# Kernel optimization log

Hardware: AMD Instinct MI355X
Metric: run time of the kernel (lower is better)

## Reference

```python
import jax, jax.numpy as jnp
import numpy as np

N, E, D, G = 50000, 600000, 128, 1024
NEG_SLOPE = 0.2  # PyG GATConv default negative_slope


def setup_inputs() -> dict:
    key = jax.random.key(0)
    ks = jax.random.split(key, 20)
    s = 1.0 / np.sqrt(D)
    inp = {
        "x": jax.random.normal(ks[0], (N, D), jnp.float32),
        "edge_index": jax.random.randint(ks[1], (2, E), 0, N, dtype=jnp.int64),
        "edge_attr": jax.random.normal(ks[2], (E, 1), jnp.float32),  # ignored (edge_dim=None)
        "batch": jnp.sort(jax.random.randint(ks[3], (N,), 0, G, dtype=jnp.int64)),
    }
    k = 4
    for name in ("g1", "g2", "g3"):
        inp[f"{name}_W"] = jax.random.normal(ks[k], (D, D), jnp.float32) * s; k += 1
        inp[f"{name}_a_src"] = jax.random.normal(ks[k], (D,), jnp.float32) * s; k += 1
        inp[f"{name}_a_dst"] = jax.random.normal(ks[k], (D,), jnp.float32) * s; k += 1
        inp[f"{name}_b"] = jnp.zeros((D,), jnp.float32)
    inp["lin_W"] = jax.random.normal(ks[k], (D, D), jnp.float32) * s
    inp["lin_b"] = jnp.zeros((D,), jnp.float32)
    return inp


def _gat(x, src, dst, W, a_src, a_dst, b):
    # PyG GATConv, heads=1: project, edge attention logits, scatter-softmax over
    # destination nodes, weighted scatter-add aggregation, plus bias.
    n = x.shape[0]
    h = x @ W                                            # [N, D]
    logits = jax.nn.leaky_relu((h @ a_src)[src] + (h @ a_dst)[dst], NEG_SLOPE)  # [E']
    m = jax.ops.segment_max(logits, dst, num_segments=n)
    p = jnp.exp(logits - m[dst])
    denom = jax.ops.segment_sum(p, dst, num_segments=n)
    alpha = p / (denom[dst] + 1e-16)                     # PyG softmax eps
    out = jax.ops.segment_sum(alpha[:, None] * h[src], dst, num_segments=n)
    return out + b


def reference(x, edge_index, edge_attr, batch,
              g1_W, g1_a_src, g1_a_dst, g1_b,
              g2_W, g2_a_src, g2_a_dst, g2_b,
              g3_W, g3_a_src, g3_a_dst, g3_b,
              lin_W, lin_b):
    n = x.shape[0]
    # GATConv default add_self_loops=True
    loop = jnp.arange(n, dtype=edge_index.dtype)
    src = jnp.concatenate([edge_index[0], loop])
    dst = jnp.concatenate([edge_index[1], loop])

    h = jax.nn.relu(_gat(x, src, dst, g1_W, g1_a_src, g1_a_dst, g1_b))
    h = jax.nn.relu(_gat(h, src, dst, g2_W, g2_a_src, g2_a_dst, g2_b))
    h = _gat(h, src, dst, g3_W, g3_a_src, g3_a_dst, g3_b)

    # global_mean_pool over graph ids
    sums = jax.ops.segment_sum(h, batch, num_segments=G)
    cnts = jax.ops.segment_sum(jnp.ones((n,), h.dtype), batch, num_segments=G)
    pooled = sums / jnp.maximum(cnts, 1.0)[:, None]
    # dropout(p=0.5) is identity in eval mode
    return pooled @ lin_W + lin_b
```

## Files before the change

### kernel.cpp

```cpp
#include <hip/hip_runtime.h>

#define D 128
typedef unsigned short ushort_t;
typedef __attribute__((ext_vector_type(8))) short bf16x8;
typedef __attribute__((ext_vector_type(4))) float f32x4;

__device__ __forceinline__ float wred_max(float v){
#pragma unroll
  for (int o = 1; o < 64; o <<= 1) v = fmaxf(v, __shfl_xor(v, o, 64));
  return v;
}
__device__ __forceinline__ float wred_sum(float v){
#pragma unroll
  for (int o = 1; o < 64; o <<= 1) v += __shfl_xor(v, o, 64);
  return v;
}
__device__ __forceinline__ unsigned short f2bf(float f){
  unsigned u = __float_as_uint(f);
  unsigned r = (u + 0x7FFFu + ((u >> 16) & 1u)) >> 16;
  return (unsigned short)r;
}
__device__ __forceinline__ float bflo(unsigned u){ return __uint_as_float(u << 16); }
__device__ __forceinline__ float bfhi(unsigned u){ return __uint_as_float(u & 0xFFFF0000u); }

__global__ __launch_bounds__(256) void k_init(const float* __restrict__ W0,
                                              const float* __restrict__ W1,
                                              const float* __restrict__ W2,
                                              ushort_t* __restrict__ Wp,
                                              int* __restrict__ cnt, int n){
  int b = blockIdx.x;
  if (b < 192){
    int wi = b >> 6;
    const float* W = wi == 0 ? W0 : (wi == 1 ? W1 : W2);
    ushort_t* dst = Wp + wi * 16384;
    int idx = (b & 63) * 256 + threadIdx.x;
    int k = idx >> 7, c = idx & 127;
    int ct = c >> 4, s = k >> 5, lane = (c & 15) | (((k >> 3) & 3) << 4), e = k & 7;
    dst[((ct * 4 + s) * 64 + lane) * 8 + e] = f2bf(W[idx]);
  } else {
    int i = (b - 192) * 256 + threadIdx.x;
    if (i < n) cnt[i] = 0;
  }
}

template<bool XF32>
__device__ __forceinline__ void gemm_body(int bid, const void* __restrict__ Av,
                                          const ushort_t* __restrict__ Wp,
                                          const float* __restrict__ a_src,
                                          const float* __restrict__ a_dst,
                                          ushort_t* __restrict__ Hbf,
                                          float* __restrict__ as_,
                                          float* __restrict__ ad_,
                                          int n){
  int tid = threadIdx.x;
  int wid = tid >> 6, l = tid & 63;
  int kg = l >> 4, cin = l & 15;
  int r0 = bid * 64 + wid * 16;
  int row_l = r0 + cin;
  if (row_l > n - 1) row_l = n - 1;

  bf16x8 ah[4], al[4];
  if (XF32){
    const float* xp = (const float*)Av + (size_t)row_l * D + kg * 8;
#pragma unroll
    for (int s = 0; s < 4; s++){
      float4 f0 = *(const float4*)(xp + s * 32);
      float4 f1 = *(const float4*)(xp + s * 32 + 4);
      float fv[8] = {f0.x, f0.y, f0.z, f0.w, f1.x, f1.y, f1.z, f1.w};
#pragma unroll
      for (int e = 0; e < 8; e++){
        unsigned short h = f2bf(fv[e]);
        ah[s][e] = (short)h;
        float r = fv[e] - __uint_as_float((unsigned)h << 16);
        al[s][e] = (short)f2bf(r);
      }
    }
  } else {
    const ushort_t* xp = (const ushort_t*)Av + (size_t)row_l * D + kg * 8;
#pragma unroll
    for (int s = 0; s < 4; s++) ah[s] = *(const bf16x8*)(xp + s * 32);
  }

  const bf16x8* Bh = (const bf16x8*)Wp;

  f32x4 acc[8];
#pragma unroll
  for (int ct = 0; ct < 8; ct++) acc[ct] = (f32x4){0.f, 0.f, 0.f, 0.f};

#pragma unroll
  for (int ct = 0; ct < 8; ct++)
#pragma unroll
    for (int s = 0; s < 4; s++){
      bf16x8 bh = Bh[(ct * 4 + s) * 64 + l];
      acc[ct] = __builtin_amdgcn_mfma_f32_16x16x32_bf16(ah[s], bh, acc[ct], 0, 0, 0);
      if (XF32)
        acc[ct] = __builtin_amdgcn_mfma_f32_16x16x32_bf16(al[s], bh, acc[ct], 0, 0, 0);
    }

  float asv[8], adv[8];
#pragma unroll
  for (int ct = 0; ct < 8; ct++){
    asv[ct] = a_src[ct * 16 + cin];
    adv[ct] = a_dst[ct * 16 + cin];
  }
#pragma unroll
  for (int j = 0; j < 4; j++){
    float ps = 0.f, pd = 0.f;
#pragma unroll
    for (int ct = 0; ct < 8; ct++){ ps += acc[ct][j] * asv[ct]; pd += acc[ct][j] * adv[ct]; }
#pragma unroll
    for (int o = 1; o < 16; o <<= 1){ ps += __shfl_xor(ps, o, 64); pd += __shfl_xor(pd, o, 64); }
    int row = r0 + kg * 4 + j;
    if (row < n){
      if (cin == 0) as_[row] = ps;
      if (cin == 1) ad_[row] = pd;
#pragma unroll
      for (int ct = 0; ct < 8; ct++)
        Hbf[(size_t)row * D + ct * 16 + cin] = f2bf(acc[ct][j]);
    }
  }
}

__global__ __launch_bounds__(256) void k_gemm_mfma_bf(const void* __restrict__ Av,
                                                      const ushort_t* __restrict__ Wp,
                                                      const float* __restrict__ a_src,
                                                      const float* __restrict__ a_dst,
                                                      ushort_t* __restrict__ Hbf,
                                                      float* __restrict__ as_,
                                                      float* __restrict__ ad_,
                                                      int n){
  gemm_body<false>(blockIdx.x, Av, Wp, a_src, a_dst, Hbf, as_, ad_, n);
}

__global__ __launch_bounds__(256) void k_gemm1_fill(const float* __restrict__ x,
                                                    const ushort_t* __restrict__ Wp,
                                                    const float* __restrict__ a_src,
                                                    const float* __restrict__ a_dst,
                                                    ushort_t* __restrict__ Hbf,
                                                    float* __restrict__ as_,
                                                    float* __restrict__ ad_,
                                                    int n, int gemm_grid,
                                                    const int* __restrict__ src,
                                                    const int* __restrict__ dst,
                                                    int E, int sliceN,
                                                    int* __restrict__ cnt,
                                                    ushort_t* __restrict__ csr_pad){
  int b = blockIdx.x;
  if (b < gemm_grid){
    gemm_body<true>(b, x, Wp, a_src, a_dst, Hbf, as_, ad_, n);
  } else {
    int f = b - gemm_grid;
    int chunk = f >> 3;
    int slice = b & 7;
    int d_lo = slice * sliceN;
    int d_hi = d_lo + sliceN;
    int e0 = chunk * 2048 + (int)threadIdx.x;
#pragma unroll
    for (int i = 0; i < 8; i++){
      int e = e0 + i * 256;
      if (e < E){
        int d = dst[e];
        if (d >= d_lo && d < d_hi){
          int s = src[e];
          int slot = atomicAdd(&cnt[d], 1);
          if (slot < 63) csr_pad[((size_t)d << 6) + slot] = (ushort_t)s;
        }
      }
    }
  }
}

template<bool OUTBF>
__global__ __launch_bounds__(256) void k_agg(const uint4* __restrict__ hb4,
                                             const ushort_t* __restrict__ csr_pad,
                                             const int* __restrict__ cnt,
                                             const float* __restrict__ asrc,
                                             const float* __restrict__ adst,
                                             const float* __restrict__ bias,
                                             ushort_t* __restrict__ outb,
                                             float* __restrict__ outf,
                                             int relu, int n){
  int node = (blockIdx.x * 256 + threadIdx.x) >> 6;
  if (node >= n) return;
  int lane = threadIdx.x & 63;
  int q = lane & 15, g = lane >> 4;
  int degr = cnt[node]; if (degr > 63) degr = 63;
  int degp = degr + 1;
  const ushort_t* eb = csr_pad + ((size_t)node << 6);
  float adn = adst[node];

  int s = node; float logit = -1e30f;
  if (lane < degr) s = eb[lane];
  if (lane <= degr){
    float xx = asrc[s] + adn;
    logit = xx >= 0.f ? xx : 0.2f * xx;
  }
  float m = wred_max(logit);
  float p = (lane <= degr) ? __expf(logit - m) : 0.f;
  float denom = wred_sum(p);
  float inv = 1.f / (denom + 1e-16f);

  float acc[8] = {0.f, 0.f, 0.f, 0.f, 0.f, 0.f, 0.f, 0.f};
#pragma unroll 2
  for (int j = 0; j < degp; j += 4){
    int slot = j + g;
    int   sj = __shfl(s, slot, 64);
    float wj = (slot < degp) ? __shfl(p, slot, 64) : 0.f;
    uint4 v = hb4[(size_t)sj * 16 + q];
    acc[0] += wj * bflo(v.x); acc[1] += wj * bfhi(v.x);
    acc[2] += wj * bflo(v.y); acc[3] += wj * bfhi(v.y);
    acc[4] += wj * bflo(v.z); acc[5] += wj * bfhi(v.z);
    acc[6] += wj * bflo(v.w); acc[7] += wj * bfhi(v.w);
  }
#pragma unroll
  for (int o = 16; o < 64; o <<= 1){
#pragma unroll
    for (int i = 0; i < 8; i++) acc[i] += __shfl_xor(acc[i], o, 64);
  }

  if (g == 0){
    float4 b0 = *(const float4*)&bias[q * 8];
    float4 b1 = *(const float4*)&bias[q * 8 + 4];
    float o0 = acc[0] * inv + b0.x, o1 = acc[1] * inv + b0.y;
    float o2 = acc[2] * inv + b0.z, o3 = acc[3] * inv + b0.w;
    float o4 = acc[4] * inv + b1.x, o5 = acc[5] * inv + b1.y;
    float o6 = acc[6] * inv + b1.z, o7 = acc[7] * inv + b1.w;
    if (relu){
      o0 = fmaxf(o0, 0.f); o1 = fmaxf(o1, 0.f); o2 = fmaxf(o2, 0.f); o3 = fmaxf(o3, 0.f);
      o4 = fmaxf(o4, 0.f); o5 = fmaxf(o5, 0.f); o6 = fmaxf(o6, 0.f); o7 = fmaxf(o7, 0.f);
    }
    if (OUTBF){
      ushort4 u0, u1;
      u0.x = f2bf(o0); u0.y = f2bf(o1); u0.z = f2bf(o2); u0.w = f2bf(o3);
      u1.x = f2bf(o4); u1.y = f2bf(o5); u1.z = f2bf(o6); u1.w = f2bf(o7);
      *(ushort4*)&outb[(size_t)node * D + q * 8]     = u0;
      *(ushort4*)&outb[(size_t)node * D + q * 8 + 4] = u1;
    } else {
      *(float4*)&outf[(size_t)node * D + q * 8]     = make_float4(o0, o1, o2, o3);
      *(float4*)&outf[(size_t)node * D + q * 8 + 4] = make_float4(o4, o5, o6, o7);
    }
  }
}

__device__ __forceinline__ int lbound(const int* a, int n, int key){
  int lo = 0, hi = n;
  while (lo < hi){ int mid = (lo + hi) >> 1; if (a[mid] < key) lo = mid + 1; else hi = mid; }
  return lo;
}

__global__ __launch_bounds__(128) void k_pool_final(const float* __restrict__ x,
                                                    const int* __restrict__ batch,
                                                    const float* __restrict__ Wl,
                                                    const float* __restrict__ bl,
                                                    float* __restrict__ out, int n){
  __shared__ float pl[128];
  int g = blockIdx.x;
  int c = threadIdx.x;
  int lo = lbound(batch, n, g);
  int hi = lbound(batch, n, g + 1);
  float sum = 0.f;
  for (int i = lo; i < hi; i++) sum += x[(size_t)i * D + c];
  float cnt = (float)(hi - lo);
  pl[c] = sum / fmaxf(cnt, 1.f);
  __syncthreads();
  float acc = bl[c];
#pragma unroll 4
  for (int k = 0; k < 128; k++) acc += pl[k] * Wl[(size_t)k * D + c];
  out[(size_t)g * D + c] = acc;
}

extern "C" void kernel_launch(void* const* d_in, const int* in_sizes, int n_in,
                              void* d_out, int out_size, void* d_ws, size_t ws_size,
                              hipStream_t stream){
  const float* x     = (const float*)d_in[0];
  const int*   ei    = (const int*)d_in[1];
  const int*   batch = (const int*)d_in[3];
  const float* gW[3]  = {(const float*)d_in[4],  (const float*)d_in[8],  (const float*)d_in[12]};
  const float* gAs[3] = {(const float*)d_in[5],  (const float*)d_in[9],  (const float*)d_in[13]};
  const float* gAd[3] = {(const float*)d_in[6],  (const float*)d_in[10], (const float*)d_in[14]};
  const float* gB[3]  = {(const float*)d_in[7],  (const float*)d_in[11], (const float*)d_in[15]};
  const float* linW = (const float*)d_in[16];
  const float* linB = (const float*)d_in[17];
  float* outp = (float*)d_out;

  int N  = in_sizes[3];
  int E  = in_sizes[1] / 2;
  int G  = out_size / D;

  char* ws = (char*)d_ws;
  size_t off = 0;
  auto alloc = [&](size_t bytes)->void*{
    void* p = ws + off;
    off += (bytes + 255) & ~(size_t)255;
    return p;
  };
  float*    bufF    = (float*)alloc((size_t)N * D * 4);
  ushort_t* bufB    = (ushort_t*)alloc((size_t)N * D * 2);
  ushort_t* Hbf     = (ushort_t*)alloc((size_t)N * D * 2);
  float*    as_     = (float*)alloc((size_t)N * 4);
  float*    ad_     = (float*)alloc((size_t)N * 4);
  int*      cnt     = (int*)  alloc((size_t)N * 4);
  ushort_t* csr_pad = (ushort_t*)alloc((size_t)N * 64 * 2);
  ushort_t* Wp      = (ushort_t*)alloc(3 * 16384 * 2);
  (void)ws_size; (void)n_in;

  const int* esrc = ei;
  const int* edst = ei + E;

  int tpb = 256;
  int ngrid = (N + tpb - 1) / tpb;
  int gemm_grid = (N + 63) / 64;
  int node_grid = (N + 3) / 4;
  int nchunk = (E + 2047) / 2048;
  int sliceN = (N + 7) / 8;

  k_init<<<192 + ngrid, tpb, 0, stream>>>(gW[0], gW[1], gW[2], Wp, cnt, N);

  const uint4* hbu = (const uint4*)Hbf;

  k_gemm1_fill<<<gemm_grid + nchunk * 8, tpb, 0, stream>>>(x, Wp, gAs[0], gAd[0], Hbf, as_, ad_, N,
                                                           gemm_grid, esrc, edst, E, sliceN, cnt, csr_pad);
  k_agg<true>  <<<node_grid, tpb, 0, stream>>>(hbu, csr_pad, cnt, as_, ad_, gB[0], bufB, nullptr, 1, N);
  k_gemm_mfma_bf<<<gemm_grid, tpb, 0, stream>>>(bufB, Wp + 16384, gAs[1], gAd[1], Hbf, as_, ad_, N);
  k_agg<true>  <<<node_grid, tpb, 0, stream>>>(hbu, csr_pad, cnt, as_, ad_, gB[1], bufB, nullptr, 1, N);
  k_gemm_mfma_bf<<<gemm_grid, tpb, 0, stream>>>(bufB, Wp + 32768, gAs[2], gAd[2], Hbf, as_, ad_, N);
  k_agg<false> <<<node_grid, tpb, 0, stream>>>(hbu, csr_pad, cnt, as_, ad_, gB[2], nullptr, bufF, 0, N);

  k_pool_final<<<G, 128, 0, stream>>>(bufF, batch, linW, linB, outp, N);
}
```

Baseline: 211.1 us.

## Reorder GAT to aggregate-then-project and fuse aggregation with GEMM

Precomputes W·a_src and W·a_dst so attention logits can be computed from layer inputs, then aggregates neighbour features before multiplying by W inside a single fused per-layer kernel. This removes the separate GEMM launches and the intermediate H buffer writes/reads, and emits next-layer logits in the epilogue. In exchange, layer 1 gathers fp32 rows (double bytes), the GEMM uses a 3-pass split-bf16 scheme, and the large shared-memory tile with serial per-wave node loops may reduce occupancy.

```diff
diff --git a/kernel.cpp b/kernel.cpp
--- a/kernel.cpp
+++ b/kernel.cpp
@@ -22,134 +22,79 @@
 }
 __device__ __forceinline__ float bflo(unsigned u){ return __uint_as_float(u << 16); }
 __device__ __forceinline__ float bfhi(unsigned u){ return __uint_as_float(u & 0xFFFF0000u); }
+__device__ __forceinline__ int lbound(const int* a, int n, int key){
+  int lo = 0, hi = n;
+  while (lo < hi){ int mid = (lo + hi) >> 1; if (a[mid] < key) lo = mid + 1; else hi = mid; }
+  return lo;
+}
 
 __global__ __launch_bounds__(256) void k_init(const float* __restrict__ W0,
                                               const float* __restrict__ W1,
                                               const float* __restrict__ W2,
+                                              const float* __restrict__ As0, const float* __restrict__ Ad0,
+                                              const float* __restrict__ As1, const float* __restrict__ Ad1,
+                                              const float* __restrict__ As2, const float* __restrict__ Ad2,
                                               ushort_t* __restrict__ Wp,
+                                              float* __restrict__ wv,
                                               int* __restrict__ cnt, int n){
   int b = blockIdx.x;
   if (b < 192){
     int wi = b >> 6;
     const float* W = wi == 0 ? W0 : (wi == 1 ? W1 : W2);
-    ushort_t* dst = Wp + wi * 16384;
+    ushort_t* dst = Wp + wi * 32768;
     int idx = (b & 63) * 256 + threadIdx.x;
     int k = idx >> 7, c = idx & 127;
+    float w = W[idx];
+    unsigned short hi = f2bf(w);
+    float r = w - __uint_as_float((unsigned)hi << 16);
     int ct = c >> 4, s = k >> 5, lane = (c & 15) | (((k >> 3) & 3) << 4), e = k & 7;
-    dst[((ct * 4 + s) * 64 + lane) * 8 + e] = f2bf(W[idx]);
+    int off = ((ct * 4 + s) * 64 + lane) * 8 + e;
+    dst[off] = hi;
+    dst[16384 + off] = f2bf(r);
+  } else if (b < 198){
+    int vi = b - 192;
+    int li = vi >> 1;
+    const float* W = li == 0 ? W0 : (li == 1 ? W1 : W2);
+    const float* a = (vi & 1) ? (li == 0 ? Ad0 : (li == 1 ? Ad1 : Ad2))
+                              : (li == 0 ? As0 : (li == 1 ? As1 : As2));
+    int t = threadIdx.x;
+    if (t < 128){
+      float acc = 0.f;
+#pragma unroll 4
+      for (int c = 0; c < 128; c++) acc += W[(size_t)t * D + c] * a[c];
+      wv[vi * 128 + t] = acc;
+    }
   } else {
-    int i = (b - 192) * 256 + threadIdx.x;
+    int i = (b - 198) * 256 + threadIdx.x;
     if (i < n) cnt[i] = 0;
   }
 }
 
-template<bool XF32>
-__device__ __forceinline__ void gemm_body(int bid, const void* __restrict__ Av,
-                                          const ushort_t* __restrict__ Wp,
-                                          const float* __restrict__ a_src,
-                                          const float* __restrict__ a_dst,
-                                          ushort_t* __restrict__ Hbf,
-                                          float* __restrict__ as_,
-                                          float* __restrict__ ad_,
-                                          int n){
-  int tid = threadIdx.x;
-  int wid = tid >> 6, l = tid & 63;
-  int kg = l >> 4, cin = l & 15;
-  int r0 = bid * 64 + wid * 16;
-  int row_l = r0 + cin;
-  if (row_l > n - 1) row_l = n - 1;
-
-  bf16x8 ah[4], al[4];
-  if (XF32){
-    const float* xp = (const float*)Av + (size_t)row_l * D + kg * 8;
-#pragma unroll
-    for (int s = 0; s < 4; s++){
-      float4 f0 = *(const float4*)(xp + s * 32);
-      float4 f1 = *(const float4*)(xp + s * 32 + 4);
-      float fv[8] = {f0.x, f0.y, f0.z, f0.w, f1.x, f1.y, f1.z, f1.w};
-#pragma unroll
-      for (int e = 0; e < 8; e++){
-        unsigned short h = f2bf(fv[e]);
-        ah[s][e] = (short)h;
-        float r = fv[e] - __uint_as_float((unsigned)h << 16);
-        al[s][e] = (short)f2bf(r);
-      }
-    }
+__global__ __launch_bounds__(256) void k_fill_dots(const float* __restrict__ x,
+                                                   const float* __restrict__ wv,
+                                                   float* __restrict__ asA,
+                                                   float* __restrict__ adA,
+                                                   int n, int dgrid,
+                                                   const int* __restrict__ src,
+                                                   const int* __restrict__ dst,
+                                                   int E, int sliceN,
+                                                   int* __restrict__ cnt,
+                                                   ushort_t* __restrict__ csr_pad){
+  int b = blockIdx.x;
+  if (b < dgrid){
+    int w = (b * 256 + (int)threadIdx.x) >> 6;
+    if (w >= n) return;
+    int lane = threadIdx.x & 63;
+    float2 hv = *(const float2*)&x[(size_t)w * D + lane * 2];
+    float2 s2 = *(const float2*)&wv[lane * 2];
+    float2 d2 = *(const float2*)&wv[128 + lane * 2];
+    float ps = hv.x * s2.x + hv.y * s2.y;
+    float pd = hv.x * d2.x + hv.y * d2.y;
+#pragma unroll
+    for (int o = 1; o < 64; o <<= 1){ ps += __shfl_xor(ps, o, 64); pd += __shfl_xor(pd, o, 64); }
+    if (lane == 0){ asA[w] = ps; adA[w] = pd; }
   } else {
-    const ushort_t* xp = (const ushort_t*)Av + (size_t)row_l * D + kg * 8;
-#pragma unroll
-    for (int s = 0; s < 4; s++) ah[s] = *(const bf16x8*)(xp + s * 32);
-  }
-
-  const bf16x8* Bh = (const bf16x8*)Wp;
-
-  f32x4 acc[8];
-#pragma unroll
-  for (int ct = 0; ct < 8; ct++) acc[ct] = (f32x4){0.f, 0.f, 0.f, 0.f};
-
-#pragma unroll
-  for (int ct = 0; ct < 8; ct++)
-#pragma unroll
-    for (int s = 0; s < 4; s++){
-      bf16x8 bh = Bh[(ct * 4 + s) * 64 + l];
-      acc[ct] = __builtin_amdgcn_mfma_f32_16x16x32_bf16(ah[s], bh, acc[ct], 0, 0, 0);
-      if (XF32)
-        acc[ct] = __builtin_amdgcn_mfma_f32_16x16x32_bf16(al[s], bh, acc[ct], 0, 0, 0);
-    }
-
-  float asv[8], adv[8];
-#pragma unroll
-  for (int ct = 0; ct < 8; ct++){
-    asv[ct] = a_src[ct * 16 + cin];
-    adv[ct] = a_dst[ct * 16 + cin];
-  }
-#pragma unroll
-  for (int j = 0; j < 4; j++){
-    float ps = 0.f, pd = 0.f;
-#pragma unroll
-    for (int ct = 0; ct < 8; ct++){ ps += acc[ct][j] * asv[ct]; pd += acc[ct][j] * adv[ct]; }
-#pragma unroll
-    for (int o = 1; o < 16; o <<= 1){ ps += __shfl_xor(ps, o, 64); pd += __shfl_xor(pd, o, 64); }
-    int row = r0 + kg * 4 + j;
-    if (row < n){
-      if (cin == 0) as_[row] = ps;
-      if (cin == 1) ad_[row] = pd;
-#pragma unroll
-      for (int ct = 0; ct < 8; ct++)
-        Hbf[(size_t)row * D + ct * 16 + cin] = f2bf(acc[ct][j]);
-    }
-  }
-}
-
-__global__ __launch_bounds__(256) void k_gemm_mfma_bf(const void* __restrict__ Av,
-                                                      const ushort_t* __restrict__ Wp,
-                                                      const float* __restrict__ a_src,
-                                                      const float* __restrict__ a_dst,
-                                                      ushort_t* __restrict__ Hbf,
-                                                      float* __restrict__ as_,
-                                                      float* __restrict__ ad_,
-                                                      int n){
-  gemm_body<false>(blockIdx.x, Av, Wp, a_src, a_dst, Hbf, as_, ad_, n);
-}
-
-__global__ __launch_bounds__(256) void k_gemm1_fill(const float* __restrict__ x,
-                                                    const ushort_t* __restrict__ Wp,
-                                                    const float* __restrict__ a_src,
-                                                    const float* __restrict__ a_dst,
-                                                    ushort_t* __restrict__ Hbf,
-                                                    float* __restrict__ as_,
-                                                    float* __restrict__ ad_,
-                                                    int n, int gemm_grid,
-                                                    const int* __restrict__ src,
-                                                    const int* __restrict__ dst,
-                                                    int E, int sliceN,
-                                                    int* __restrict__ cnt,
-                                                    ushort_t* __restrict__ csr_pad){
-  int b = blockIdx.x;
-  if (b < gemm_grid){
-    gemm_body<true>(b, x, Wp, a_src, a_dst, Hbf, as_, ad_, n);
-  } else {
-    int f = b - gemm_grid;
+    int f = b - dgrid;
     int chunk = f >> 3;
     int slice = b & 7;
     int d_lo = slice * sliceN;
@@ -170,82 +115,145 @@
   }
 }
 
-template<bool OUTBF>
-__global__ __launch_bounds__(256) void k_agg(const uint4* __restrict__ hb4,
-                                             const ushort_t* __restrict__ csr_pad,
-                                             const int* __restrict__ cnt,
-                                             const float* __restrict__ asrc,
-                                             const float* __restrict__ adst,
-                                             const float* __restrict__ bias,
-                                             ushort_t* __restrict__ outb,
-                                             float* __restrict__ outf,
-                                             int relu, int n){
-  int node = (blockIdx.x * 256 + threadIdx.x) >> 6;
-  if (node >= n) return;
-  int lane = threadIdx.x & 63;
-  int q = lane & 15, g = lane >> 4;
-  int degr = cnt[node]; if (degr > 63) degr = 63;
-  int degp = degr + 1;
-  const ushort_t* eb = csr_pad + ((size_t)node << 6);
-  float adn = adst[node];
-
-  int s = node; float logit = -1e30f;
-  if (lane < degr) s = eb[lane];
-  if (lane <= degr){
-    float xx = asrc[s] + adn;
-    logit = xx >= 0.f ? xx : 0.2f * xx;
-  }
-  float m = wred_max(logit);
-  float p = (lane <= degr) ? __expf(logit - m) : 0.f;
-  float denom = wred_sum(p);
-  float inv = 1.f / (denom + 1e-16f);
-
-  float acc[8] = {0.f, 0.f, 0.f, 0.f, 0.f, 0.f, 0.f, 0.f};
+template<int MODE>
+__global__ __launch_bounds__(256) void k_layer(const void* __restrict__ Xin,
+                                               const ushort_t* __restrict__ Wp,
+                                               const float* __restrict__ as_cur,
+                                               const float* __restrict__ ad_cur,
+                                               const float* __restrict__ wv_next,
+                                               const float* __restrict__ bias,
+                                               ushort_t* __restrict__ outb,
+                                               float* __restrict__ outf,
+                                               float* __restrict__ as_next,
+                                               float* __restrict__ ad_next,
+                                               const ushort_t* __restrict__ csr_pad,
+                                               const int* __restrict__ cnt, int n){
+  __shared__ float zsh[64][132];
+  int tid = (int)threadIdx.x;
+  int w = tid >> 6, l = tid & 63;
+  int q = l & 15, g = l >> 4;
+  int nb0 = blockIdx.x * 64;
+
+  for (int i = 0; i < 16; i++){
+    int node = nb0 + w * 16 + i;
+    float acc[8] = {0.f, 0.f, 0.f, 0.f, 0.f, 0.f, 0.f, 0.f};
+    float inv = 0.f;
+    if (node < n){
+      int degr = cnt[node]; if (degr > 63) degr = 63;
+      int degp = degr + 1;
+      const ushort_t* eb = csr_pad + ((size_t)node << 6);
+      float adn = ad_cur[node];
+      int s = node; float logit = -1e30f;
+      if (l < degr) s = eb[l];
+      if (l <= degr){
+        float xx = as_cur[s] + adn;
+        logit = xx >= 0.f ? xx : 0.2f * xx;
+      }
+      float m = wred_max(logit);
+      float p = (l <= degr) ? __expf(logit - m) : 0.f;
+      float denom = wred_sum(p);
+      inv = 1.f / (denom + 1e-16f);
 #pragma unroll 2
-  for (int j = 0; j < degp; j += 4){
-    int slot = j + g;
-    int   sj = __shfl(s, slot, 64);
-    float wj = (slot < degp) ? __shfl(p, slot, 64) : 0.f;
-    uint4 v = hb4[(size_t)sj * 16 + q];
-    acc[0] += wj * bflo(v.x); acc[1] += wj * bfhi(v.x);
-    acc[2] += wj * bflo(v.y); acc[3] += wj * bfhi(v.y);
-    acc[4] += wj * bflo(v.z); acc[5] += wj * bfhi(v.z);
-    acc[6] += wj * bflo(v.w); acc[7] += wj * bfhi(v.w);
-  }
-#pragma unroll
-  for (int o = 16; o < 64; o <<= 1){
-#pragma unroll
-    for (int i = 0; i < 8; i++) acc[i] += __shfl_xor(acc[i], o, 64);
-  }
-
-  if (g == 0){
-    float4 b0 = *(const float4*)&bias[q * 8];
-    float4 b1 = *(const float4*)&bias[q * 8 + 4];
-    float o0 = acc[0] * inv + b0.x, o1 = acc[1] * inv + b0.y;
-    float o2 = acc[2] * inv + b0.z, o3 = acc[3] * inv + b0.w;
-    float o4 = acc[4] * inv + b1.x, o5 = acc[5] * inv + b1.y;
-    float o6 = acc[6] * inv + b1.z, o7 = acc[7] * inv + b1.w;
-    if (relu){
-      o0 = fmaxf(o0, 0.f); o1 = fmaxf(o1, 0.f); o2 = fmaxf(o2, 0.f); o3 = fmaxf(o3, 0.f);
-      o4 = fmaxf(o4, 0.f); o5 = fmaxf(o5, 0.f); o6 = fmaxf(o6, 0.f); o7 = fmaxf(o7, 0.f);
-    }
-    if (OUTBF){
-      ushort4 u0, u1;
-      u0.x = f2bf(o0); u0.y = f2bf(o1); u0.z = f2bf(o2); u0.w = f2bf(o3);
-      u1.x = f2bf(o4); u1.y = f2bf(o5); u1.z = f2bf(o6); u1.w = f2bf(o7);
-      *(ushort4*)&outb[(size_t)node * D + q * 8]     = u0;
-      *(ushort4*)&outb[(size_t)node * D + q * 8 + 4] = u1;
-    } else {
-      *(float4*)&outf[(size_t)node * D + q * 8]     = make_float4(o0, o1, o2, o3);
-      *(float4*)&outf[(size_t)node * D + q * 8 + 4] = make_float4(o4, o5, o6, o7);
-    }
-  }
-}
-
-__device__ __forceinline__ int lbound(const int* a, int n, int key){
-  int lo = 0, hi = n;
-  while (lo < hi){ int mid = (lo + hi) >> 1; if (a[mid] < key) lo = mid + 1; else hi = mid; }
-  return lo;
+      for (int j = 0; j < degp; j += 4){
+        int slot = j + g;
+        int   sj = __shfl(s, slot, 64);
+        float wj = (slot < degp) ? __shfl(p, slot, 64) : 0.f;
+        if (MODE == 0){
+          const float4* xr = (const float4*)Xin + (size_t)sj * 32 + q * 2;
+          float4 v0 = xr[0], v1 = xr[1];
+          acc[0] += wj * v0.x; acc[1] += wj * v0.y; acc[2] += wj * v0.z; acc[3] += wj * v0.w;
+          acc[4] += wj * v1.x; acc[5] += wj * v1.y; acc[6] += wj * v1.z; acc[7] += wj * v1.w;
+        } else {
+          uint4 v = ((const uint4*)Xin)[(size_t)sj * 16 + q];
+          acc[0] += wj * bflo(v.x); acc[1] += wj * bfhi(v.x);
+          acc[2] += wj * bflo(v.y); acc[3] += wj * bfhi(v.y);
+          acc[4] += wj * bflo(v.z); acc[5] += wj * bfhi(v.z);
+          acc[6] += wj * bflo(v.w); acc[7] += wj * bfhi(v.w);
+        }
+      }
+#pragma unroll
+      for (int o = 16; o < 64; o <<= 1){
+#pragma unroll
+        for (int ii = 0; ii < 8; ii++) acc[ii] += __shfl_xor(acc[ii], o, 64);
+      }
+    }
+    if (g == 0){
+      float4 z0 = make_float4(acc[0] * inv, acc[1] * inv, acc[2] * inv, acc[3] * inv);
+      float4 z1 = make_float4(acc[4] * inv, acc[5] * inv, acc[6] * inv, acc[7] * inv);
+      *(float4*)&zsh[w * 16 + i][q * 8]     = z0;
+      *(float4*)&zsh[w * 16 + i][q * 8 + 4] = z1;
+    }
+  }
+  __syncthreads();
+
+  int kg = l >> 4, cin = l & 15;
+  bf16x8 ah[4], al[4];
+#pragma unroll
+  for (int s = 0; s < 4; s++){
+    const float4* zr = (const float4*)&zsh[w * 16 + cin][s * 32 + kg * 8];
+    float4 f0 = zr[0], f1 = zr[1];
+    float fv[8] = {f0.x, f0.y, f0.z, f0.w, f1.x, f1.y, f1.z, f1.w};
+#pragma unroll
+    for (int e = 0; e < 8; e++){
+      unsigned short h = f2bf(fv[e]);
+      ah[s][e] = (short)h;
+      al[s][e] = (short)f2bf(fv[e] - __uint_as_float((unsigned)h << 16));
+    }
+  }
+
+  const bf16x8* Bh = (const bf16x8*)Wp;
+  const bf16x8* Bl = (const bf16x8*)(Wp + 16384);
+  f32x4 accc[8];
+#pragma unroll
+  for (int ct = 0; ct < 8; ct++) accc[ct] = (f32x4){0.f, 0.f, 0.f, 0.f};
+#pragma unroll
+  for (int ct = 0; ct < 8; ct++)
+#pragma unroll
+    for (int s = 0; s < 4; s++){
+      bf16x8 bh = Bh[(ct * 4 + s) * 64 + l];
+      bf16x8 bl = Bl[(ct * 4 + s) * 64 + l];
+      accc[ct] = __builtin_amdgcn_mfma_f32_16x16x32_bf16(ah[s], bh, accc[ct], 0, 0, 0);
+      accc[ct] = __builtin_amdgcn_mfma_f32_16x16x32_bf16(al[s], bh, accc[ct], 0, 0, 0);
+      accc[ct] = __builtin_amdgcn_mfma_f32_16x16x32_bf16(ah[s], bl, accc[ct], 0, 0, 0);
+    }
+
+  float bv[8], wsn[8], wdn[8];
+#pragma unroll
+  for (int ct = 0; ct < 8; ct++){
+    bv[ct] = bias[ct * 16 + cin];
+    if (MODE != 2){
+      wsn[ct] = wv_next[ct * 16 + cin];
+      wdn[ct] = wv_next[128 + ct * 16 + cin];
+    }
+  }
+#pragma unroll
+  for (int j = 0; j < 4; j++){
+    int row = nb0 + w * 16 + kg * 4 + j;
+    float o[8];
+#pragma unroll
+    for (int ct = 0; ct < 8; ct++){
+      float v = accc[ct][j] + bv[ct];
+      if (MODE != 2) v = fmaxf(v, 0.f);
+      o[ct] = v;
+    }
+    if (MODE != 2){
+      float ps = 0.f, pd = 0.f;
+#pragma unroll
+      for (int ct = 0; ct < 8; ct++){ ps += o[ct] * wsn[ct]; pd += o[ct] * wdn[ct]; }
+#pragma unroll
+      for (int of = 1; of < 16; of <<= 1){ ps += __shfl_xor(ps, of, 64); pd += __shfl_xor(pd, of, 64); }
+      if (row < n && cin == 0){ as_next[row] = ps; ad_next[row] = pd; }
+    }
+    if (row < n){
+      if (MODE == 2){
+#pragma unroll
+        for (int ct = 0; ct < 8; ct++) outf[(size_t)row * D + ct * 16 + cin] = o[ct];
+      } else {
+#pragma unroll
+        for (int ct = 0; ct < 8; ct++) outb[(size_t)row * D + ct * 16 + cin] = f2bf(o[ct]);
+      }
+    }
+  }
 }
 
 __global__ __launch_bounds__(128) void k_pool_final(const float* __restrict__ x,
@@ -295,13 +303,18 @@
     return p;
   };
   float*    bufF    = (float*)alloc((size_t)N * D * 4);
-  ushort_t* bufB    = (ushort_t*)alloc((size_t)N * D * 2);
-  ushort_t* Hbf     = (ushort_t*)alloc((size_t)N * D * 2);
-  float*    as_     = (float*)alloc((size_t)N * 4);
-  float*    ad_     = (float*)alloc((size_t)N * 4);
+  ushort_t* X2      = (ushort_t*)alloc((size_t)N * D * 2);
+  ushort_t* X3      = (ushort_t*)alloc((size_t)N * D * 2);
+  float*    asA     = (float*)alloc((size_t)N * 4);
+  float*    adA     = (float*)alloc((size_t)N * 4);
+  float*    asB     = (float*)alloc((size_t)N * 4);
+  float*    adB     = (float*)alloc((size_t)N * 4);
+  float*    asC     = (float*)alloc((size_t)N * 4);
+  float*    adC     = (float*)alloc((size_t)N * 4);
   int*      cnt     = (int*)  alloc((size_t)N * 4);
   ushort_t* csr_pad = (ushort_t*)alloc((size_t)N * 64 * 2);
-  ushort_t* Wp      = (ushort_t*)alloc(3 * 16384 * 2);
+  ushort_t* Wp      = (ushort_t*)alloc(3 * 2 * 16384 * 2);
+  float*    wv      = (float*)alloc(6 * 128 * 4);
   (void)ws_size; (void)n_in;
 
   const int* esrc = ei;
@@ -309,22 +322,21 @@
 
   int tpb = 256;
   int ngrid = (N + tpb - 1) / tpb;
-  int gemm_grid = (N + 63) / 64;
-  int node_grid = (N + 3) / 4;
+  int layer_grid = (N + 63) / 64;
+  int dgrid = (N + 3) / 4;
   int nchunk = (E + 2047) / 2048;
   int sliceN = (N + 7) / 8;
 
-  k_init<<<192 + ngrid, tpb, 0, stream>>>(gW[0], gW[1], gW[2], Wp, cnt, N);
-
-  const uint4* hbu = (const uint4*)Hbf;
-
-  k_gemm1_fill<<<gemm_grid + nchunk * 8, tpb, 0, stream>>>(x, Wp, gAs[0], gAd[0], Hbf, as_, ad_, N,
-                                                           gemm_grid, esrc, edst, E, sliceN, cnt, csr_pad);
-  k_agg<true>  <<<node_grid, tpb, 0, stream>>>(hbu, csr_pad, cnt, as_, ad_, gB[0], bufB, nullptr, 1, N);
-  k_gemm_mfma_bf<<<gemm_grid, tpb, 0, stream>>>(bufB, Wp + 16384, gAs[1], gAd[1], Hbf, as_, ad_, N);
-  k_agg<true>  <<<node_grid, tpb, 0, stream>>>(hbu, csr_pad, cnt, as_, ad_, gB[1], bufB, nullptr, 1, N);
-  k_gemm_mfma_bf<<<gemm_grid, tpb, 0, stream>>>(bufB, Wp + 32768, gAs[2], gAd[2], Hbf, as_, ad_, N);
-  k_agg<false> <<<node_grid, tpb, 0, stream>>>(hbu, csr_pad, cnt, as_, ad_, gB[2], nullptr, bufF, 0, N);
-
+  k_init<<<198 + ngrid, tpb, 0, stream>>>(gW[0], gW[1], gW[2],
+                                          gAs[0], gAd[0], gAs[1], gAd[1], gAs[2], gAd[2],
+                                          Wp, wv, cnt, N);
+  k_fill_dots<<<dgrid + nchunk * 8, tpb, 0, stream>>>(x, wv, asA, adA, N, dgrid,
+                                                      esrc, edst, E, sliceN, cnt, csr_pad);
+  k_layer<0><<<layer_grid, tpb, 0, stream>>>(x, Wp, asA, adA, wv + 2 * 128, gB[0],
+                                             X2, nullptr, asB, adB, csr_pad, cnt, N);
+  k_layer<1><<<layer_grid, tpb, 0, stream>>>(X2, Wp + 2 * 16384, asB, adB, wv + 4 * 128, gB[1],
+                                             X3, nullptr, asC, adC, csr_pad, cnt, N);
+  k_layer<2><<<layer_grid, tpb, 0, stream>>>(X3, Wp + 4 * 16384, asC, adC, wv, gB[2],
+                                             nullptr, bufF, nullptr, nullptr, csr_pad, cnt, N);
   k_pool_final<<<G, 128, 0, stream>>>(bufF, batch, linW, linB, outp, N);
 }
```

New measurement: 269.3 us. +27.6%, slower.
